# Kernel tuning notes

Measured on AMD Instinct MI355X. Metric: run time of the kernel, lower is better.

Reference implementation:

```python
import jax, jax.numpy as jnp
import numpy as np

NUM_FRAMES = 36
NUM_QUERIES = 36000            # num_out = 1000
NUM_TGT = 256                  # flat targets = NUM_TGT * NUM_FRAMES = 9216
NUM_CLASSES = 81
COST_CLASS = 1.0
COST_BBOX = 1.0
COST_GIOU = 1.0


def box_cxcywh_to_xyxy(b):
    cx, cy, w, h = b[..., 0], b[..., 1], b[..., 2], b[..., 3]
    return jnp.stack([cx - 0.5 * w, cy - 0.5 * h, cx + 0.5 * w, cy + 0.5 * h], axis=-1)


def multi_giou(a, b):
    # elementwise (broadcasted) generalized IoU over last-dim xyxy boxes
    lt = jnp.maximum(a[..., :2], b[..., :2])
    rb = jnp.minimum(a[..., 2:], b[..., 2:])
    wh = jnp.clip(rb - lt, 0.0)
    inter = wh[..., 0] * wh[..., 1]
    area_a = (a[..., 2] - a[..., 0]) * (a[..., 3] - a[..., 1])
    area_b = (b[..., 2] - b[..., 0]) * (b[..., 3] - b[..., 1])
    union = area_a + area_b - inter
    iou = inter / union
    lt_c = jnp.minimum(a[..., :2], b[..., :2])
    rb_c = jnp.maximum(a[..., 2:], b[..., 2:])
    wh_c = jnp.clip(rb_c - lt_c, 0.0)
    area_c = wh_c[..., 0] * wh_c[..., 1]
    return iou - (area_c - union) / area_c


def setup_inputs() -> dict:
    key = jax.random.key(0)
    k1, k2, k3, k4 = jax.random.split(key, 4)
    pred_logits = jax.random.normal(k1, (NUM_QUERIES, NUM_CLASSES), dtype=jnp.float32)
    pred_boxes = jax.random.uniform(k2, (NUM_QUERIES, 4), dtype=jnp.float32,
                                    minval=0.05, maxval=0.95)
    tgt_bbox = jax.random.uniform(k3, (NUM_TGT * NUM_FRAMES, 4), dtype=jnp.float32,
                                  minval=0.05, maxval=0.95)
    tgt_ids = jax.random.randint(k4, (NUM_TGT * NUM_FRAMES,), 0, NUM_CLASSES)
    return {
        "pred_logits": pred_logits,
        "pred_boxes": pred_boxes,
        "tgt_bbox": tgt_bbox,
        "tgt_ids": tgt_ids,
        "num_frames": NUM_FRAMES,
    }


def reference(pred_logits, pred_boxes, tgt_bbox, tgt_ids, num_frames):
    Q, C = pred_logits.shape
    F = num_frames
    O = Q // F                      # num_out (queries per frame / tracks)
    T = tgt_ids.shape[0] // F       # num targets (tracks)

    out_prob = jax.nn.softmax(pred_logits, axis=-1)
    # [F, O, C] -> [O, F, C]
    out_prob_split = jnp.transpose(out_prob.reshape(F, O, C), (1, 0, 2))
    # gather over (frame, class) pairs: frame_index repeats 0..F-1 per target
    frame_index = jnp.tile(jnp.arange(F), T)          # [T*F]
    class_cost = -out_prob_split[:, frame_index, tgt_ids]      # [O, T*F]
    class_cost = class_cost.reshape(O, T, F).mean(axis=-1)     # [O, T]

    # [O, 1, F, 4] vs [1, T, F, 4]
    out_bbox_split = jnp.transpose(pred_boxes.reshape(F, O, 4), (1, 0, 2))[:, None]
    tgt_bbox_split = tgt_bbox.reshape(T, F, 4)[None]
    bbox_cost = jnp.abs(out_bbox_split - tgt_bbox_split).mean(axis=(-1, -2))  # [O, T]

    giou = multi_giou(box_cxcywh_to_xyxy(out_bbox_split),
                      box_cxcywh_to_xyxy(tgt_bbox_split))       # [O, T, F]
    iou_cost = -giou.mean(axis=-1)                              # [O, T]

    cost = COST_CLASS * class_cost + COST_BBOX * bbox_cost + COST_GIOU * iou_cost
    return cost
```

## Files before the change

### kernel.cpp

```cpp
#include <hip/hip_runtime.h>
#include <hip/hip_bf16.h>

#define NF 36
#define NO 1000
#define NT 256
#define NC 81

#define NROWS (NF * NO)
#define SM_BLOCKS (NROWS / 4)
#define TP_BLOCKS ((NF * NT + 255) / 256)

#define WS_BYTES (NF * NT * 16 + NROWS * NC * 4 + (NF / 4) * NT * 4)

__global__ __launch_bounds__(256) void matcher_prep_kernel(
    const float* __restrict__ logits,
    const float* __restrict__ tboxes,
    const int*   __restrict__ tids,
    float*  __restrict__ prob_ws,
    float4* __restrict__ tb_x,
    uchar4* __restrict__ pk)
{
    const int b = blockIdx.x;
    if (b < SM_BLOCKS) {
        const int wave = threadIdx.x >> 6;
        const int lane = threadIdx.x & 63;
        const int r = b * 4 + wave;
        const int f = r / NO;
        const int o = r - f * NO;
        const float* row = logits + (size_t)r * NC;
        float e1 = (lane      < NC) ? __expf(row[lane])      : 0.0f;
        float e2 = (lane + 64 < NC) ? __expf(row[lane + 64]) : 0.0f;
        float s = e1 + e2;
        #pragma unroll
        for (int m = 32; m; m >>= 1) s += __shfl_xor(s, m);
        const float inv = __builtin_amdgcn_rcpf(s);
        float* dst = prob_ws + (size_t)o * (NF * NC) + f * NC;
        if (lane      < NC) dst[lane]      = e1 * inv;
        if (lane + 64 < NC) dst[lane + 64] = e2 * inv;
    } else {
        const int i = (b - SM_BLOCKS) * 256 + threadIdx.x;
        if (i < NF * NT) {
            const int f = i / NT, t = i - f * NT;
            const float4 bb = ((const float4*)tboxes)[t * NF + f];
            float4 x;
            x.x = bb.x - 0.5f * bb.z;  x.y = bb.y - 0.5f * bb.w;
            x.z = bb.x + 0.5f * bb.z;  x.w = bb.y + 0.5f * bb.w;
            tb_x[i] = x;
        }
        if (i < (NF / 4) * NT) {
            const int fb4 = i / NT, t = i - fb4 * NT;
            const int4 v = *(const int4*)(tids + t * NF + fb4 * 4);
            uchar4 u;
            u.x = (unsigned char)v.x;  u.y = (unsigned char)v.y;
            u.z = (unsigned char)v.z;  u.w = (unsigned char)v.w;
            pk[i] = u;
        }
    }
}

__global__ __launch_bounds__(256, 4) void matcher_main_kernel(
    const float* __restrict__ pboxes,
    const float* __restrict__ prob_ws,
    const float4* __restrict__ tb_x,
    const uchar4* __restrict__ pk,
    float* __restrict__ out)
{
    const int o   = blockIdx.x;
    const int tid = threadIdx.x;

    __shared__ float  prob[NF * NC];
    __shared__ float4 pbx[NF];
    __shared__ float  pbarea[NF];

    {
        const float4* src = (const float4*)(prob_ws + (size_t)o * (NF * NC));
        float4* dst = (float4*)prob;
        #pragma unroll
        for (int i = tid; i < (NF * NC) / 4; i += 256) dst[i] = src[i];
    }
    if (tid < NF) {
        const float4 pc = ((const float4*)pboxes)[tid * NO + o];
        float4 x;
        x.x = pc.x - 0.5f * pc.z;  x.y = pc.y - 0.5f * pc.w;
        x.z = pc.x + 0.5f * pc.z;  x.w = pc.y + 0.5f * pc.w;
        pbx[tid] = x;
        pbarea[tid] = pc.z * pc.w;
    }
    __syncthreads();

    const int t = tid;
    float acc_cls = 0.0f, acc_l1 = 0.0f, acc_giou = 0.0f;

    #pragma unroll 2
    for (int fb = 0; fb < NF; fb += 4) {
        const uchar4 c4 = pk[(fb >> 2) * NT + t];
        float4 tx[4];
        #pragma unroll
        for (int j = 0; j < 4; ++j) tx[j] = tb_x[(fb + j) * NT + t];
        const int cls[4] = {c4.x, c4.y, c4.z, c4.w};

        #pragma unroll
        for (int j = 0; j < 4; ++j) {
            const int f = fb + j;
            const float4 tv = tx[j];
            const float4 pb = pbx[f];

            acc_cls += prob[f * NC + cls[j]];

            const float dx0 = pb.x - tv.x, dy0 = pb.y - tv.y;
            const float dx1 = pb.z - tv.z, dy1 = pb.w - tv.w;
            acc_l1 += 0.5f * (fabsf(dx0 + dx1) + fabsf(dy0 + dy1))
                    + fabsf(dx1 - dx0) + fabsf(dy1 - dy0);

            const float ltx = fmaxf(pb.x, tv.x), lty = fmaxf(pb.y, tv.y);
            const float rbx = fminf(pb.z, tv.z), rby = fminf(pb.w, tv.w);
            const float inter = fmaxf(rbx - ltx, 0.0f) * fmaxf(rby - lty, 0.0f);

            const float area_b = (tv.z - tv.x) * (tv.w - tv.y);
            const float uni = pbarea[f] + area_b - inter;

            const float cx0 = fminf(pb.x, tv.x), cy0 = fminf(pb.y, tv.y);
            const float cx1 = fmaxf(pb.z, tv.z), cy1 = fmaxf(pb.w, tv.w);
            const float area_c = (cx1 - cx0) * (cy1 - cy0);

            acc_giou += inter * __builtin_amdgcn_rcpf(uni)
                      - (area_c - uni) * __builtin_amdgcn_rcpf(area_c);
        }
    }

    const float inv_f  = 1.0f / (float)NF;
    const float inv_4f = 1.0f / (float)(4 * NF);
    out[(size_t)o * NT + t] = -acc_cls * inv_f + acc_l1 * inv_4f - acc_giou * inv_f;
}

__global__ __launch_bounds__(256) void matcher_fallback_kernel(
    const float* __restrict__ logits, const float* __restrict__ pboxes,
    const float* __restrict__ tboxes, const int* __restrict__ tids,
    float* __restrict__ out)
{
    const int o = blockIdx.x, tid = threadIdx.x;
    const int wave = tid >> 6, lane = tid & 63;
    __shared__ float prob[NF * NC];
    __shared__ float pb[NF][4];
    for (int f = wave; f < NF; f += 4) {
        const float* row = logits + (size_t)(f * NO + o) * NC;
        float e1 = (lane < NC) ? __expf(row[lane]) : 0.0f;
        float e2 = (lane + 64 < NC) ? __expf(row[lane + 64]) : 0.0f;
        float s = e1 + e2;
        #pragma unroll
        for (int m = 32; m; m >>= 1) s += __shfl_xor(s, m);
        const float inv = 1.0f / s;
        if (lane < NC)      prob[f * NC + lane]      = e1 * inv;
        if (lane + 64 < NC) prob[f * NC + lane + 64] = e2 * inv;
    }
    if (tid < NF * 4) {
        const int f = tid >> 2, k = tid & 3;
        pb[f][k] = pboxes[(size_t)(f * NO + o) * 4 + k];
    }
    __syncthreads();
    const int t = tid;
    const float4* tb4 = (const float4*)tboxes;
    float acc_cls = 0.0f, acc_l1 = 0.0f, acc_giou = 0.0f;
    for (int f = 0; f < NF; ++f) {
        const int cls = tids[t * NF + f];
        const float4 tb = tb4[t * NF + f];
        acc_cls += prob[f * NC + cls];
        const float pcx = pb[f][0], pcy = pb[f][1], pw = pb[f][2], ph = pb[f][3];
        acc_l1 += fabsf(pcx - tb.x) + fabsf(pcy - tb.y) + fabsf(pw - tb.z) + fabsf(ph - tb.w);
        const float ax0 = pcx - 0.5f * pw, ay0 = pcy - 0.5f * ph;
        const float ax1 = pcx + 0.5f * pw, ay1 = pcy + 0.5f * ph;
        const float bx0 = tb.x - 0.5f * tb.z, by0 = tb.y - 0.5f * tb.w;
        const float bx1 = tb.x + 0.5f * tb.z, by1 = tb.y + 0.5f * tb.w;
        const float ltx = fmaxf(ax0, bx0), lty = fmaxf(ay0, by0);
        const float rbx = fminf(ax1, bx1), rby = fminf(ay1, by1);
        const float inter = fmaxf(rbx - ltx, 0.0f) * fmaxf(rby - lty, 0.0f);
        const float uni = (ax1 - ax0) * (ay1 - ay0) + (bx1 - bx0) * (by1 - by0) - inter;
        const float cx0 = fminf(ax0, bx0), cy0 = fminf(ay0, by0);
        const float cx1 = fmaxf(ax1, bx1), cy1 = fmaxf(ay1, by1);
        const float area_c = fmaxf(cx1 - cx0, 0.0f) * fmaxf(cy1 - cy0, 0.0f);
        acc_giou += inter / uni - (area_c - uni) / area_c;
    }
    out[(size_t)o * NT + t] = (-acc_cls - acc_giou) * (1.0f / NF) + acc_l1 * (1.0f / (4 * NF));
}

extern "C" void kernel_launch(void* const* d_in, const int* in_sizes, int n_in,
                              void* d_out, int out_size, void* d_ws, size_t ws_size,
                              hipStream_t stream) {
    const float* pred_logits = (const float*)d_in[0];
    const float* pred_boxes  = (const float*)d_in[1];
    const float* tgt_bbox    = (const float*)d_in[2];
    const int*   tgt_ids     = (const int*)d_in[3];
    float* out = (float*)d_out;

    if (ws_size >= (size_t)WS_BYTES) {
        float4* tb_x    = (float4*)d_ws;
        float*  prob_ws = (float*)(tb_x + NF * NT);
        uchar4* pk      = (uchar4*)(prob_ws + (size_t)NROWS * NC);
        matcher_prep_kernel<<<SM_BLOCKS + TP_BLOCKS, 256, 0, stream>>>(
            pred_logits, tgt_bbox, tgt_ids, prob_ws, tb_x, pk);
        matcher_main_kernel<<<NO, 256, 0, stream>>>(
            pred_boxes, prob_ws, tb_x, pk, out);
    } else {
        matcher_fallback_kernel<<<NO, 256, 0, stream>>>(
            pred_logits, pred_boxes, tgt_bbox, tgt_ids, out);
    }
}
```

Baseline: 91.40 us.

## Split frame loop across four thread groups with shared-memory reduction

```diff
diff --git a/kernel.cpp b/kernel.cpp
--- a/kernel.cpp
+++ b/kernel.cpp
@@ -10,7 +10,7 @@
 #define SM_BLOCKS (NROWS / 4)
 #define TP_BLOCKS ((NF * NT + 255) / 256)
 
-#define WS_BYTES (NF * NT * 16 + NROWS * NC * 4 + (NF / 4) * NT * 4)
+#define WS_BYTES (NF * NT * 16 + NROWS * NC * 4 + NF * NT)
 
 __global__ __launch_bounds__(256) void matcher_prep_kernel(
     const float* __restrict__ logits,
@@ -18,7 +18,7 @@
     const int*   __restrict__ tids,
     float*  __restrict__ prob_ws,
     float4* __restrict__ tb_x,
-    uchar4* __restrict__ pk)
+    unsigned char* __restrict__ ids_u8)
 {
     const int b = blockIdx.x;
     if (b < SM_BLOCKS) {
@@ -46,37 +46,32 @@
             x.x = bb.x - 0.5f * bb.z;  x.y = bb.y - 0.5f * bb.w;
             x.z = bb.x + 0.5f * bb.z;  x.w = bb.y + 0.5f * bb.w;
             tb_x[i] = x;
-        }
-        if (i < (NF / 4) * NT) {
-            const int fb4 = i / NT, t = i - fb4 * NT;
-            const int4 v = *(const int4*)(tids + t * NF + fb4 * 4);
-            uchar4 u;
-            u.x = (unsigned char)v.x;  u.y = (unsigned char)v.y;
-            u.z = (unsigned char)v.z;  u.w = (unsigned char)v.w;
-            pk[i] = u;
+            ids_u8[i] = (unsigned char)tids[t * NF + f];
         }
     }
 }
 
-__global__ __launch_bounds__(256, 4) void matcher_main_kernel(
+__global__ __launch_bounds__(1024) void matcher_main_kernel(
     const float* __restrict__ pboxes,
     const float* __restrict__ prob_ws,
     const float4* __restrict__ tb_x,
-    const uchar4* __restrict__ pk,
+    const unsigned char* __restrict__ ids_u8,
     float* __restrict__ out)
 {
     const int o   = blockIdx.x;
     const int tid = threadIdx.x;
+    const int t   = tid & (NT - 1);
+    const int fg  = tid >> 8;
 
     __shared__ float  prob[NF * NC];
     __shared__ float4 pbx[NF];
     __shared__ float  pbarea[NF];
+    __shared__ float  red[4 * NT];
 
     {
         const float4* src = (const float4*)(prob_ws + (size_t)o * (NF * NC));
         float4* dst = (float4*)prob;
-        #pragma unroll
-        for (int i = tid; i < (NF * NC) / 4; i += 256) dst[i] = src[i];
+        if (tid < (NF * NC) / 4) dst[tid] = src[tid];
     }
     if (tid < NF) {
         const float4 pc = ((const float4*)pboxes)[tid * NO + o];
@@ -88,49 +83,46 @@
     }
     __syncthreads();
 
-    const int t = tid;
     float acc_cls = 0.0f, acc_l1 = 0.0f, acc_giou = 0.0f;
+    const int f0 = fg * 9;
 
-    #pragma unroll 2
-    for (int fb = 0; fb < NF; fb += 4) {
-        const uchar4 c4 = pk[(fb >> 2) * NT + t];
-        float4 tx[4];
-        #pragma unroll
-        for (int j = 0; j < 4; ++j) tx[j] = tb_x[(fb + j) * NT + t];
-        const int cls[4] = {c4.x, c4.y, c4.z, c4.w};
+    #pragma unroll 3
+    for (int k = 0; k < 9; ++k) {
+        const int f = f0 + k;
+        const int cls = ids_u8[f * NT + t];
+        const float4 tv = tb_x[f * NT + t];
+        const float4 pb = pbx[f];
 
-        #pragma unroll
-        for (int j = 0; j < 4; ++j) {
-            const int f = fb + j;
-            const float4 tv = tx[j];
-            const float4 pb = pbx[f];
+        acc_cls += prob[f * NC + cls];
 
-            acc_cls += prob[f * NC + cls[j]];
+        const float dx0 = pb.x - tv.x, dy0 = pb.y - tv.y;
+        const float dx1 = pb.z - tv.z, dy1 = pb.w - tv.w;
+        acc_l1 += 0.5f * (fabsf(dx0 + dx1) + fabsf(dy0 + dy1))
+                + fabsf(dx1 - dx0) + fabsf(dy1 - dy0);
 
-            const float dx0 = pb.x - tv.x, dy0 = pb.y - tv.y;
-            const float dx1 = pb.z - tv.z, dy1 = pb.w - tv.w;
-            acc_l1 += 0.5f * (fabsf(dx0 + dx1) + fabsf(dy0 + dy1))
-                    + fabsf(dx1 - dx0) + fabsf(dy1 - dy0);
+        const float ltx = fmaxf(pb.x, tv.x), lty = fmaxf(pb.y, tv.y);
+        const float rbx = fminf(pb.z, tv.z), rby = fminf(pb.w, tv.w);
+        const float inter = fmaxf(rbx - ltx, 0.0f) * fmaxf(rby - lty, 0.0f);
 
-            const float ltx = fmaxf(pb.x, tv.x), lty = fmaxf(pb.y, tv.y);
-            const float rbx = fminf(pb.z, tv.z), rby = fminf(pb.w, tv.w);
-            const float inter = fmaxf(rbx - ltx, 0.0f) * fmaxf(rby - lty, 0.0f);
+        const float area_b = (tv.z - tv.x) * (tv.w - tv.y);
+        const float uni = pbarea[f] + area_b - inter;
 
-            const float area_b = (tv.z - tv.x) * (tv.w - tv.y);
-            const float uni = pbarea[f] + area_b - inter;
+        const float cx0 = fminf(pb.x, tv.x), cy0 = fminf(pb.y, tv.y);
+        const float cx1 = fmaxf(pb.z, tv.z), cy1 = fmaxf(pb.w, tv.w);
+        const float area_c = (cx1 - cx0) * (cy1 - cy0);
 
-            const float cx0 = fminf(pb.x, tv.x), cy0 = fminf(pb.y, tv.y);
-            const float cx1 = fmaxf(pb.z, tv.z), cy1 = fmaxf(pb.w, tv.w);
-            const float area_c = (cx1 - cx0) * (cy1 - cy0);
-
-            acc_giou += inter * __builtin_amdgcn_rcpf(uni)
-                      - (area_c - uni) * __builtin_amdgcn_rcpf(area_c);
-        }
+        acc_giou += inter * __builtin_amdgcn_rcpf(uni)
+                  - (area_c - uni) * __builtin_amdgcn_rcpf(area_c);
     }
 
     const float inv_f  = 1.0f / (float)NF;
     const float inv_4f = 1.0f / (float)(4 * NF);
-    out[(size_t)o * NT + t] = -acc_cls * inv_f + acc_l1 * inv_4f - acc_giou * inv_f;
+    red[fg * NT + t] = -(acc_cls + acc_giou) * inv_f + acc_l1 * inv_4f;
+    __syncthreads();
+
+    if (tid < NT)
+        out[(size_t)o * NT + tid] = (red[tid] + red[NT + tid])
+                                  + (red[2 * NT + tid] + red[3 * NT + tid]);
 }
 
 __global__ __launch_bounds__(256) void matcher_fallback_kernel(
@@ -195,11 +187,11 @@
     if (ws_size >= (size_t)WS_BYTES) {
         float4* tb_x    = (float4*)d_ws;
         float*  prob_ws = (float*)(tb_x + NF * NT);
-        uchar4* pk      = (uchar4*)(prob_ws + (size_t)NROWS * NC);
+        unsigned char* ids_u8 = (unsigned char*)(prob_ws + (size_t)NROWS * NC);
         matcher_prep_kernel<<<SM_BLOCKS + TP_BLOCKS, 256, 0, stream>>>(
-            pred_logits, tgt_bbox, tgt_ids, prob_ws, tb_x, pk);
-        matcher_main_kernel<<<NO, 256, 0, stream>>>(
-            pred_boxes, prob_ws, tb_x, pk, out);
+            pred_logits, tgt_bbox, tgt_ids, prob_ws, tb_x, ids_u8);
+        matcher_main_kernel<<<NO, 1024, 0, stream>>>(
+            pred_boxes, prob_ws, tb_x, ids_u8, out);
     } else {
         matcher_fallback_kernel<<<NO, 256, 0, stream>>>(
             pred_logits, pred_boxes, tgt_bbox, tgt_ids, out);
```

Result: no change. 91.16 us (-0.3%).
